# Optimization experiments

Measured on AMD Instinct MI355X. Metric: run time of the kernel, lower is better.

The kernel has to match this reference:

```python
import jax, jax.numpy as jnp
import numpy as np

M, C, D = 262144, 91, 256
MOMENTUM = 0.999
WARMUP = 200
TAU = 0.1
REP_COEF = 0.1


def _l2(x):
    # F.normalize(dim=-1): x / max(||x||, 1e-12)
    return x / jnp.clip(jnp.linalg.norm(x, axis=-1, keepdims=True), 1e-12)


def setup_inputs() -> dict:
    key = jax.random.key(0)
    k = jax.random.split(key, 5)
    return {
        "features": jax.random.normal(k[0], (M, D), jnp.float32),
        "labels": jax.random.randint(k[1], (M,), 0, C, jnp.int32),
        "prototypes": jax.random.normal(k[2], (C, D), jnp.float32),
        "proto_initialized": jnp.ones((C,), jnp.bool_),
        "proto_update_count": jax.random.randint(k[3], (C,), 0, 1000, jnp.int32),
        "proto_variance": jax.random.uniform(k[4], (C,), jnp.float32, minval=0.1, maxval=2.0),
        "step": 500,
    }


def reference(features, labels, prototypes, proto_initialized, proto_update_count, proto_variance, step):
    num_classes = prototypes.shape[0]
    # ---------- update(): no-grad EMA prototype scatter-update ----------
    fdet = _l2(jax.lax.stop_gradient(features))  # (M, D)
    seg_sum = jax.ops.segment_sum(fdet, labels, num_segments=num_classes)          # (C, D)
    cnt = jax.ops.segment_sum(jnp.ones((fdet.shape[0],), jnp.float32), labels,
                              num_segments=num_classes)                            # (C,)
    has = cnt > 0
    cls_mean = seg_sum / jnp.maximum(cnt, 1.0)[:, None]                            # per-class mean feature
    # adaptive momentum ramp 0.99 -> MOMENTUM over 10*warmup steps
    progress = min(1.0, float(step) / max(1, WARMUP * 10))
    m = 0.99 + (MOMENTUM - 0.99) * progress
    ema = m * prototypes + (1.0 - m) * cls_mean
    new_proto = jnp.where(has[:, None],
                          jnp.where(proto_initialized[:, None], ema, cls_mean),
                          prototypes)
    update_mag = jnp.linalg.norm(cls_mean - prototypes, axis=-1)                   # (C,)
    upd = has & proto_initialized
    new_var = jnp.where(upd, 0.99 * proto_variance + 0.01 * update_mag, proto_variance)
    new_cnt = proto_update_count + has.astype(proto_update_count.dtype)
    new_init = proto_initialized | has

    # ---------- loss(): pull (weighted CE on cosine logits) + repulsion ----------
    valid = new_init[labels]                                                       # (M,)
    vm = valid.astype(jnp.float32)
    nv = jnp.maximum(vm.sum(), 1e-8)

    def mmean(x):  # mean over valid subset
        return (x * vm).sum() / nv

    feats_norm = _l2(features)                                                     # (M, D)
    protos_norm = _l2(new_proto)                                                   # (C, D)
    logits = feats_norm @ protos_norm.T / TAU                                      # (M, C)
    loss_per = -jax.nn.log_softmax(logits, axis=-1)[jnp.arange(logits.shape[0]), labels]

    freq = 1.0 / jnp.maximum(new_cnt[labels].astype(jnp.float32), 1.0)
    freq = jnp.minimum(freq / jnp.maximum(mmean(freq), 1e-8), 5.0)
    qual = 1.0 / jnp.maximum(new_var[labels], 1e-4)
    qual = jnp.minimum(qual / jnp.maximum(mmean(qual), 1e-8), 5.0)
    w = freq * qual
    w = w / jnp.maximum(mmean(w), 1e-8)
    pull = mmean(loss_per * w)

    sim = protos_norm @ protos_norm.T                                              # (C, C)
    tri = jnp.triu(jnp.ones_like(sim, dtype=bool), k=1) & new_init[:, None] & new_init[None, :]
    npairs = tri.sum().astype(jnp.float32)
    rep = jnp.where(npairs > 0,
                    (jnp.maximum(sim, 0.0) * tri).sum() / jnp.maximum(npairs, 1.0),
                    0.0)
    return pull + REP_COEF * rep
```

## Files before the change

### kernel.cpp

```cpp
#include <hip/hip_runtime.h>
#include <hip/hip_bf16.h>
#include <math.h>
#include <stdint.h>

#define CDIM 91
#define DDIM 256
#define CPAD 96
#define NFRAG 24576

typedef float f32x4 __attribute__((ext_vector_type(4)));
typedef short v8s   __attribute__((ext_vector_type(8)));

__device__ __forceinline__ float wave_sum(float v) {
    #pragma unroll
    for (int off = 32; off > 0; off >>= 1)
        v += __shfl_xor(v, off, 64);
    return v;
}

__device__ __forceinline__ float block_sum128(volatile float* red, int t, float v) {
    red[t] = v;
    __syncthreads();
    for (int s = 64; s > 0; s >>= 1) {
        if (t < s) red[t] += red[t + s];
        __syncthreads();
    }
    float r = red[0];
    __syncthreads();
    return r;
}

__device__ __forceinline__ unsigned short f2bf(float x) {
    union { float f; unsigned u; } a; a.f = x;
    unsigned r = a.u + 0x7fff + ((a.u >> 16) & 1);
    return (unsigned short)(r >> 16);
}
__device__ __forceinline__ float bf2f(unsigned short h) {
    union { unsigned u; float f; } a; a.u = ((unsigned)h) << 16; return a.f;
}

__global__ __launch_bounds__(1024) void k1_fused(
    const float* __restrict__ f, const int* __restrict__ labels,
    float* __restrict__ inv, unsigned int* __restrict__ cnt,
    float* __restrict__ seg, int M)
{
    __shared__ float acc[CDIM * DDIM];
    __shared__ unsigned int hist[CDIM];
    for (int t = threadIdx.x; t < CDIM * DDIM; t += 1024) acc[t] = 0.0f;
    if (threadIdx.x < CDIM) hist[threadIdx.x] = 0;
    __syncthreads();
    const int sub  = threadIdx.x >> 6;
    const int lane = threadIdx.x & 63;
    const int rows = M / gridDim.x;
    const int r0 = blockIdx.x * rows, r1 = r0 + rows;
    for (int r = r0 + sub; r < r1; r += 16) {
        const float* frow = f + (size_t)r * DDIM;
        const float v0 = frow[lane], v1 = frow[lane + 64];
        const float v2 = frow[lane + 128], v3 = frow[lane + 192];
        const float ss = wave_sum(v0*v0 + v1*v1 + v2*v2 + v3*v3);
        const float iv = 1.0f / fmaxf(sqrtf(ss), 1e-12f);
        const int c = labels[r];
        if (lane == 0) { inv[r] = iv; atomicAdd(&hist[c], 1u); }
        float* a = acc + c * DDIM;
        atomicAdd(a + lane,       v0 * iv);
        atomicAdd(a + lane + 64,  v1 * iv);
        atomicAdd(a + lane + 128, v2 * iv);
        atomicAdd(a + lane + 192, v3 * iv);
    }
    __syncthreads();
    for (int i = threadIdx.x; i < CDIM * DDIM; i += 1024)
        unsafeAtomicAdd(&seg[i], acc[i]);
    if (threadIdx.x < CDIM && hist[threadIdx.x])
        atomicAdd(&cnt[threadIdx.x], hist[threadIdx.x]);
}

__global__ __launch_bounds__(256) void k2_update(
    const float* __restrict__ seg, const unsigned int* __restrict__ cnt,
    const float* __restrict__ proto, const int* __restrict__ pinit,
    const int* __restrict__ pcount, const float* __restrict__ pvar,
    const int* __restrict__ stepp,
    float* __restrict__ pn, float* __restrict__ ncnt, float* __restrict__ nvar,
    int* __restrict__ ninit)
{
    const int wid = threadIdx.x >> 6, lane = threadIdx.x & 63;
    const int c = blockIdx.x * 4 + wid;
    if (c >= CDIM) return;
    const int d0 = lane * 4;
    const float4 s = *reinterpret_cast<const float4*>(seg + c * DDIM + d0);
    const float4 p = *reinterpret_cast<const float4*>(proto + c * DDIM + d0);
    const float cntf = (float)cnt[c];
    const bool has  = cntf > 0.0f;
    const bool init = pinit[c] != 0;
    const double prog = fmin(1.0, (double)stepp[0] / 2000.0);
    const double md = 0.99 + (0.999 - 0.99) * prog;
    const float m  = (float)md, om = (float)(1.0 - md);
    const float dn = fmaxf(cntf, 1.0f);
    const float mx = s.x / dn, my = s.y / dn, mz = s.z / dn, mw = s.w / dn;
    const float ex = m * p.x + om * mx, ey = m * p.y + om * my;
    const float ez = m * p.z + om * mz, ew = m * p.w + om * mw;
    const float nx = has ? (init ? ex : mx) : p.x;
    const float ny = has ? (init ? ey : my) : p.y;
    const float nz = has ? (init ? ez : mz) : p.z;
    const float nw = has ? (init ? ew : mw) : p.w;
    const float dx = mx - p.x, dy = my - p.y, dz = mz - p.z, dw = mw - p.w;
    const float dsum = wave_sum(dx*dx + dy*dy + dz*dz + dw*dw);
    const float nsum = wave_sum(nx*nx + ny*ny + nz*nz + nw*nw);
    const float mag = sqrtf(dsum);
    const float nrm = fmaxf(sqrtf(nsum), 1e-12f);
    float4 o; o.x = nx/nrm; o.y = ny/nrm; o.z = nz/nrm; o.w = nw/nrm;
    *reinterpret_cast<float4*>(pn + c * DDIM + d0) = o;
    if (lane == 0) {
        ncnt[c]  = (float)(pcount[c] + (has ? 1 : 0));
        nvar[c]  = (has && init) ? (0.99f * pvar[c] + 0.01f * mag) : pvar[c];
        ninit[c] = (init || has) ? 1 : 0;
    }
}

__global__ __launch_bounds__(64) void k2b_bfrag(
    const float* __restrict__ pn, unsigned short* __restrict__ bf)
{
    const int t = blockIdx.x >> 3, s = blockIdx.x & 7;
    const int l = threadIdx.x;
    const int c = t * 16 + (l & 15);
    const int k0 = s * 32 + (l >> 4) * 8;
    float v[8];
    if (c < CDIM) {
        const float4 x = *reinterpret_cast<const float4*>(pn + c * DDIM + k0);
        const float4 y = *reinterpret_cast<const float4*>(pn + c * DDIM + k0 + 4);
        v[0]=x.x; v[1]=x.y; v[2]=x.z; v[3]=x.w; v[4]=y.x; v[5]=y.y; v[6]=y.z; v[7]=y.w;
    } else {
        #pragma unroll
        for (int j = 0; j < 8; ++j) v[j] = 0.0f;
    }
    union { unsigned short u[8]; v8s vv; } H, L;
    #pragma unroll
    for (int j = 0; j < 8; ++j) {
        H.u[j] = f2bf(v[j]);
        L.u[j] = f2bf(v[j] - bf2f(H.u[j]));
    }
    const int base = ((t * 8 + s) * 64 + l) * 8;
    *reinterpret_cast<v8s*>(bf + base)         = H.vv;
    *reinterpret_cast<v8s*>(bf + NFRAG + base) = L.vv;
}

__global__ __launch_bounds__(128) void k3_weights(
    const unsigned int* __restrict__ cnt, const float* __restrict__ ncnt,
    const float* __restrict__ nvar, const int* __restrict__ ninit,
    float* __restrict__ wv, float* __restrict__ nvp, float* __restrict__ npr)
{
    __shared__ float red[128];
    const int t = threadIdx.x;
    float n_c = 0.0f, fc = 0.0f, qc = 0.0f, validc = 0.0f, initc = 0.0f;
    if (t < CDIM) {
        n_c = (float)cnt[t];
        initc = ninit[t] ? 1.0f : 0.0f;
        validc = initc;
        fc = 1.0f / fmaxf(ncnt[t], 1.0f);
        qc = 1.0f / fmaxf(nvar[t], 1e-4f);
    }
    const float nv    = fmaxf(block_sum128(red, t, n_c * validc), 1e-8f);
    const float meanf = block_sum128(red, t, n_c * validc * fc) / nv;
    const float meanq = block_sum128(red, t, n_c * validc * qc) / nv;
    const float fn = fminf(fc / fmaxf(meanf, 1e-8f), 5.0f);
    const float qn = fminf(qc / fmaxf(meanq, 1e-8f), 5.0f);
    const float w  = fn * qn;
    const float meanw = block_sum128(red, t, n_c * validc * w) / nv;
    const float wn = w / fmaxf(meanw, 1e-8f);
    if (t < CDIM) wv[t] = wn * validc;
    const float ki = block_sum128(red, t, initc);
    if (t == 0) { nvp[0] = nv; npr[0] = ki * (ki - 1.0f) * 0.5f; }
}

__global__ __launch_bounds__(256) void k4_rep(
    const float* __restrict__ pn, const int* __restrict__ ninit,
    float* __restrict__ reps)
{
    const int wid = threadIdx.x >> 6, lane = threadIdx.x & 63;
    const int gw = blockIdx.x * 4 + wid;
    const int nw = gridDim.x * 4;
    for (int p = gw; p < CDIM * CDIM; p += nw) {
        const int i = p / CDIM, j = p % CDIM;
        if (i >= j) continue;
        if (!(ninit[i] && ninit[j])) continue;
        const float4 a = *reinterpret_cast<const float4*>(pn + i * DDIM + lane * 4);
        const float4 b = *reinterpret_cast<const float4*>(pn + j * DDIM + lane * 4);
        float d = a.x*b.x + a.y*b.y + a.z*b.z + a.w*b.w;
        d = wave_sum(d);
        if (lane == 0) unsafeAtomicAdd(reps, fmaxf(d, 0.0f));
    }
}

__global__ __launch_bounds__(1024) void k5_mfma(
    const float* __restrict__ f, const int* __restrict__ labels,
    const unsigned short* __restrict__ bfg, const float* __restrict__ inv,
    const float* __restrict__ wv, float* __restrict__ pull, int M)
{
    __shared__ __align__(16) unsigned short bl[2 * NFRAG];
    {
        const float4* src = reinterpret_cast<const float4*>(bfg);
        float4* dst = reinterpret_cast<float4*>(bl);
        #pragma unroll
        for (int i = 0; i < 6; ++i)
            dst[threadIdx.x + i * 1024] = src[threadIdx.x + i * 1024];
    }
    __syncthreads();
    const int w = threadIdx.x >> 6, lane = threadIdx.x & 63;
    const int col0 = lane & 15, grp = lane >> 4;
    const int ntiles = M / 256;
    float contrib = 0.0f;

    for (int tile = blockIdx.x; tile < ntiles; tile += gridDim.x) {
        const int r0 = tile * 256 + w * 16;
        const float* frow = f + (size_t)(r0 + col0) * DDIM + grp * 8;
        f32x4 acc0 = {0,0,0,0}, acc1 = {0,0,0,0}, acc2 = {0,0,0,0};
        f32x4 acc3 = {0,0,0,0}, acc4 = {0,0,0,0}, acc5 = {0,0,0,0};
        #pragma unroll
        for (int s = 0; s < 8; ++s) {
            const float4 x = *reinterpret_cast<const float4*>(frow + s * 32);
            const float4 y = *reinterpret_cast<const float4*>(frow + s * 32 + 4);
            const float v[8] = {x.x, x.y, x.z, x.w, y.x, y.y, y.z, y.w};
            union { unsigned short u[8]; v8s vv; } AH, AL;
            #pragma unroll
            for (int j = 0; j < 8; ++j) {
                AH.u[j] = f2bf(v[j]);
                AL.u[j] = f2bf(v[j] - bf2f(AH.u[j]));
            }
            #pragma unroll
            for (int t = 0; t < 6; ++t) {
                const int off = ((t * 8 + s) * 64 + lane) * 8;
                const v8s BH = *reinterpret_cast<const v8s*>(bl + off);
                const v8s BL = *reinterpret_cast<const v8s*>(bl + NFRAG + off);
                f32x4 a = (t==0)?acc0:(t==1)?acc1:(t==2)?acc2:(t==3)?acc3:(t==4)?acc4:acc5;
                a = __builtin_amdgcn_mfma_f32_16x16x32_bf16(AH.vv, BH, a, 0, 0, 0);
                a = __builtin_amdgcn_mfma_f32_16x16x32_bf16(AH.vv, BL, a, 0, 0, 0);
                a = __builtin_amdgcn_mfma_f32_16x16x32_bf16(AL.vv, BH, a, 0, 0, 0);
                if (t==0) acc0=a; else if (t==1) acc1=a; else if (t==2) acc2=a;
                else if (t==3) acc3=a; else if (t==4) acc4=a; else acc5=a;
            }
        }
        const int rbase = r0 + grp * 4;
        const float4 invv = *reinterpret_cast<const float4*>(inv + rbase);
        const int4   labv = *reinterpret_cast<const int4*>(labels + rbase);
        #pragma unroll
        for (int rg = 0; rg < 4; ++rg) {
            const float scale = ((const float*)&invv)[rg] * 10.0f;
            const int   lab   = ((const int*)&labv)[rg];
            float v[6];
            v[0]=acc0[rg]*scale; v[1]=acc1[rg]*scale; v[2]=acc2[rg]*scale;
            v[3]=acc3[rg]*scale; v[4]=acc4[rg]*scale; v[5]=acc5[rg]*scale;
            if (col0 >= 11) v[5] = -1e30f;
            float mx = v[0];
            #pragma unroll
            for (int t = 1; t < 6; ++t) mx = fmaxf(mx, v[t]);
            #pragma unroll
            for (int o = 1; o < 16; o <<= 1) mx = fmaxf(mx, __shfl_xor(mx, o, 64));
            float se = 0.0f, ll = 0.0f;
            #pragma unroll
            for (int t = 0; t < 6; ++t) {
                se += __expf(v[t] - mx);
                if (t * 16 + col0 == lab) ll = v[t];
            }
            #pragma unroll
            for (int o = 1; o < 16; o <<= 1) {
                se += __shfl_xor(se, o, 64);
                ll += __shfl_xor(ll, o, 64);
            }
            if (col0 == 0) contrib += (mx + __logf(se) - ll) * wv[lab];
        }
    }
    contrib = wave_sum(contrib);
    if (lane == 0) unsafeAtomicAdd(pull, contrib);
}

__global__ void k6_final(const float* __restrict__ pull, const float* __restrict__ nvp,
                         const float* __restrict__ reps, const float* __restrict__ npr,
                         float* __restrict__ out)
{
    const float np = npr[0];
    const float rep = (np > 0.0f) ? (reps[0] / fmaxf(np, 1.0f)) : 0.0f;
    out[0] = pull[0] / nvp[0] + 0.1f * rep;
}

extern "C" void kernel_launch(void* const* d_in, const int* in_sizes, int n_in,
                              void* d_out, int out_size, void* d_ws, size_t ws_size,
                              hipStream_t stream)
{
    const float* features = (const float*)d_in[0];
    const int*   labels   = (const int*)d_in[1];
    const float* proto    = (const float*)d_in[2];
    const int*   pinit    = (const int*)d_in[3];
    const int*   pcount   = (const int*)d_in[4];
    const float* pvar     = (const float*)d_in[5];
    const int*   stepp    = (const int*)d_in[6];
    float*       out      = (float*)d_out;
    const int M = in_sizes[0] / DDIM;

    float* W = (float*)d_ws;
    float*        seg  = W;
    unsigned int* cnt  = (unsigned int*)(seg + CDIM * DDIM);
    float*        pull = (float*)(cnt + CDIM);
    float*        reps = pull + 1;
    float*        pn   = W + 23392;
    float*        inv  = pn + CDIM * DDIM;
    float*        wv   = inv + M;
    float*        ncnt = wv + CDIM;
    float*        nvar = ncnt + CDIM;
    float*        nvp  = nvar + CDIM;
    float*        npr  = nvp + 1;
    int*          nini = (int*)(npr + 1);
    unsigned short* bfrag = (unsigned short*)
        (((uintptr_t)(nini + CDIM) + 255) & ~(uintptr_t)255);

    hipMemsetAsync(seg, 0, (CDIM * DDIM + CDIM + 2) * sizeof(float), stream);

    k1_fused<<<256, 1024, 0, stream>>>(features, labels, inv, cnt, seg, M);
    k2_update<<<(CDIM + 3) / 4, 256, 0, stream>>>(seg, cnt, proto, pinit, pcount,
                                                  pvar, stepp, pn, ncnt, nvar, nini);
    k2b_bfrag<<<48, 64, 0, stream>>>(pn, bfrag);
    k3_weights<<<1, 128, 0, stream>>>(cnt, ncnt, nvar, nini, wv, nvp, npr);
    k4_rep<<<64, 256, 0, stream>>>(pn, nini, reps);
    k5_mfma<<<256, 1024, 0, stream>>>(features, labels, bfrag, inv, wv, pull, M);
    k6_final<<<1, 1, 0, stream>>>(pull, nvp, reps, npr, out);
}
```

Before: 1.138 ms.

## Unroll k1 rows by four and replace global seg atomics with partial-buffer reduction

The row loop in k1 now handles four rows per wave per iteration and batches their norm reductions into one interleaved shuffle tree, giving more loads in flight. The final per-block flush of 91x256 floats via global atomics is replaced, when the workspace is large enough, by plain stores into per-block partial buffers that a new reduce kernel sums. Launch bounds gain a min-blocks hint on k1 and k5. This adds about 24 MB of partial-buffer write and read traffic plus an extra launch, and the loop now hardcodes 16 iterations of 64 rows, which assumes M/256 equals 1024.

```diff
diff --git a/kernel.cpp b/kernel.cpp
--- a/kernel.cpp
+++ b/kernel.cpp
@@ -7,6 +7,7 @@
 #define DDIM 256
 #define CPAD 96
 #define NFRAG 24576
+#define SEGN (CDIM * DDIM)
 
 typedef float f32x4 __attribute__((ext_vector_type(4)));
 typedef short v8s   __attribute__((ext_vector_type(8)));
@@ -18,6 +19,16 @@
     return v;
 }
 
+__device__ __forceinline__ void wave_sum4(float& a, float& b, float& c, float& d) {
+    #pragma unroll
+    for (int off = 32; off > 0; off >>= 1) {
+        a += __shfl_xor(a, off, 64);
+        b += __shfl_xor(b, off, 64);
+        c += __shfl_xor(c, off, 64);
+        d += __shfl_xor(d, off, 64);
+    }
+}
+
 __device__ __forceinline__ float block_sum128(volatile float* red, int t, float v) {
     red[t] = v;
     __syncthreads();
@@ -39,39 +50,78 @@
     union { unsigned u; float f; } a; a.u = ((unsigned)h) << 16; return a.f;
 }
 
-__global__ __launch_bounds__(1024) void k1_fused(
+__global__ __launch_bounds__(1024, 4) void k1_fused(
     const float* __restrict__ f, const int* __restrict__ labels,
     float* __restrict__ inv, unsigned int* __restrict__ cnt,
-    float* __restrict__ seg, int M)
-{
-    __shared__ float acc[CDIM * DDIM];
+    float* __restrict__ seg, float* __restrict__ part, int usePart, int M)
+{
+    __shared__ float acc[SEGN];
     __shared__ unsigned int hist[CDIM];
-    for (int t = threadIdx.x; t < CDIM * DDIM; t += 1024) acc[t] = 0.0f;
+    for (int t = threadIdx.x; t < SEGN; t += 1024) acc[t] = 0.0f;
     if (threadIdx.x < CDIM) hist[threadIdx.x] = 0;
     __syncthreads();
-    const int sub  = threadIdx.x >> 6;
-    const int lane = threadIdx.x & 63;
-    const int rows = M / gridDim.x;
-    const int r0 = blockIdx.x * rows, r1 = r0 + rows;
-    for (int r = r0 + sub; r < r1; r += 16) {
-        const float* frow = f + (size_t)r * DDIM;
-        const float v0 = frow[lane], v1 = frow[lane + 64];
-        const float v2 = frow[lane + 128], v3 = frow[lane + 192];
-        const float ss = wave_sum(v0*v0 + v1*v1 + v2*v2 + v3*v3);
-        const float iv = 1.0f / fmaxf(sqrtf(ss), 1e-12f);
-        const int c = labels[r];
-        if (lane == 0) { inv[r] = iv; atomicAdd(&hist[c], 1u); }
-        float* a = acc + c * DDIM;
-        atomicAdd(a + lane,       v0 * iv);
-        atomicAdd(a + lane + 64,  v1 * iv);
-        atomicAdd(a + lane + 128, v2 * iv);
-        atomicAdd(a + lane + 192, v3 * iv);
-    }
-    __syncthreads();
-    for (int i = threadIdx.x; i < CDIM * DDIM; i += 1024)
-        unsafeAtomicAdd(&seg[i], acc[i]);
+    const int sub = threadIdx.x >> 6, lane = threadIdx.x & 63;
+    const int r0 = blockIdx.x * (M / gridDim.x);
+    for (int j = 0; j < 16; ++j) {
+        const int base = r0 + sub + 64 * j;
+        const float* fA = f + (size_t)base * DDIM;
+        const float* fB = fA + 16 * DDIM;
+        const float* fC = fA + 32 * DDIM;
+        const float* fD = fA + 48 * DDIM;
+        const float a0 = fA[lane], a1 = fA[lane+64], a2 = fA[lane+128], a3 = fA[lane+192];
+        const float b0 = fB[lane], b1 = fB[lane+64], b2 = fB[lane+128], b3 = fB[lane+192];
+        const float c0 = fC[lane], c1 = fC[lane+64], c2 = fC[lane+128], c3 = fC[lane+192];
+        const float d0 = fD[lane], d1 = fD[lane+64], d2 = fD[lane+128], d3 = fD[lane+192];
+        float sA = a0*a0 + a1*a1 + a2*a2 + a3*a3;
+        float sB = b0*b0 + b1*b1 + b2*b2 + b3*b3;
+        float sC = c0*c0 + c1*c1 + c2*c2 + c3*c3;
+        float sD = d0*d0 + d1*d1 + d2*d2 + d3*d3;
+        wave_sum4(sA, sB, sC, sD);
+        const float ivA = 1.0f / fmaxf(sqrtf(sA), 1e-12f);
+        const float ivB = 1.0f / fmaxf(sqrtf(sB), 1e-12f);
+        const float ivC = 1.0f / fmaxf(sqrtf(sC), 1e-12f);
+        const float ivD = 1.0f / fmaxf(sqrtf(sD), 1e-12f);
+        const int cA = labels[base],      cB = labels[base + 16];
+        const int cC = labels[base + 32], cD = labels[base + 48];
+        if (lane == 0) {
+            inv[base] = ivA; inv[base+16] = ivB; inv[base+32] = ivC; inv[base+48] = ivD;
+            atomicAdd(&hist[cA], 1u); atomicAdd(&hist[cB], 1u);
+            atomicAdd(&hist[cC], 1u); atomicAdd(&hist[cD], 1u);
+        }
+        float* pA = acc + cA * DDIM + lane;
+        atomicAdd(pA,       a0 * ivA); atomicAdd(pA + 64,  a1 * ivA);
+        atomicAdd(pA + 128, a2 * ivA); atomicAdd(pA + 192, a3 * ivA);
+        float* pB = acc + cB * DDIM + lane;
+        atomicAdd(pB,       b0 * ivB); atomicAdd(pB + 64,  b1 * ivB);
+        atomicAdd(pB + 128, b2 * ivB); atomicAdd(pB + 192, b3 * ivB);
+        float* pC = acc + cC * DDIM + lane;
+        atomicAdd(pC,       c0 * ivC); atomicAdd(pC + 64,  c1 * ivC);
+        atomicAdd(pC + 128, c2 * ivC); atomicAdd(pC + 192, c3 * ivC);
+        float* pD = acc + cD * DDIM + lane;
+        atomicAdd(pD,       d0 * ivD); atomicAdd(pD + 64,  d1 * ivD);
+        atomicAdd(pD + 128, d2 * ivD); atomicAdd(pD + 192, d3 * ivD);
+    }
+    __syncthreads();
+    if (usePart) {
+        float* dst = part + (size_t)blockIdx.x * SEGN;
+        for (int i = threadIdx.x; i < SEGN; i += 1024) dst[i] = acc[i];
+    } else {
+        for (int i = threadIdx.x; i < SEGN; i += 1024) unsafeAtomicAdd(&seg[i], acc[i]);
+    }
     if (threadIdx.x < CDIM && hist[threadIdx.x])
         atomicAdd(&cnt[threadIdx.x], hist[threadIdx.x]);
+}
+
+__global__ __launch_bounds__(256) void k1b_reduce(
+    const float* __restrict__ part, float* __restrict__ seg)
+{
+    const int i = (blockIdx.x >> 3) * 256 + threadIdx.x;
+    const int b0 = (blockIdx.x & 7) * 32;
+    float s = 0.0f;
+    #pragma unroll 8
+    for (int b = b0; b < b0 + 32; ++b)
+        s += part[(size_t)b * SEGN + i];
+    unsafeAtomicAdd(&seg[i], s);
 }
 
 __global__ __launch_bounds__(256) void k2_update(
@@ -190,7 +240,7 @@
     }
 }
 
-__global__ __launch_bounds__(1024) void k5_mfma(
+__global__ __launch_bounds__(1024, 4) void k5_mfma(
     const float* __restrict__ f, const int* __restrict__ labels,
     const unsigned short* __restrict__ bfg, const float* __restrict__ inv,
     const float* __restrict__ wv, float* __restrict__ pull, int M)
@@ -297,11 +347,11 @@
 
     float* W = (float*)d_ws;
     float*        seg  = W;
-    unsigned int* cnt  = (unsigned int*)(seg + CDIM * DDIM);
+    unsigned int* cnt  = (unsigned int*)(seg + SEGN);
     float*        pull = (float*)(cnt + CDIM);
     float*        reps = pull + 1;
     float*        pn   = W + 23392;
-    float*        inv  = pn + CDIM * DDIM;
+    float*        inv  = pn + SEGN;
     float*        wv   = inv + M;
     float*        ncnt = wv + CDIM;
     float*        nvar = ncnt + CDIM;
@@ -310,10 +360,17 @@
     int*          nini = (int*)(npr + 1);
     unsigned short* bfrag = (unsigned short*)
         (((uintptr_t)(nini + CDIM) + 255) & ~(uintptr_t)255);
-
-    hipMemsetAsync(seg, 0, (CDIM * DDIM + CDIM + 2) * sizeof(float), stream);
-
-    k1_fused<<<256, 1024, 0, stream>>>(features, labels, inv, cnt, seg, M);
+    float* part = (float*)
+        (((uintptr_t)(bfrag + 2 * NFRAG) + 255) & ~(uintptr_t)255);
+    const size_t part_bytes = (size_t)256 * SEGN * sizeof(float);
+    const size_t part_off   = (size_t)((char*)part - (char*)d_ws);
+    const int usePart = (ws_size >= part_off + part_bytes) ? 1 : 0;
+
+    hipMemsetAsync(seg, 0, (SEGN + CDIM + 2) * sizeof(float), stream);
+
+    k1_fused<<<256, 1024, 0, stream>>>(features, labels, inv, cnt, seg, part, usePart, M);
+    if (usePart)
+        k1b_reduce<<<728, 256, 0, stream>>>(part, seg);
     k2_update<<<(CDIM + 3) / 4, 256, 0, stream>>>(seg, cnt, proto, pinit, pcount,
                                                   pvar, stepp, pn, ncnt, nvar, nini);
     k2b_bfrag<<<48, 64, 0, stream>>>(pn, bfrag);
```

After: 1.107 ms. -2.7%, faster.
